# Kernel tuning notes

Measured on AMD Instinct MI355X. Metric: run time of the kernel, lower is better.

Reference implementation:

```python
import jax, jax.numpy as jnp
import numpy as np

N_NODES = 50000


def gcn_conv(x, W, b, src, dst, n):
    """PyG GCNConv: add self-loops, sym-normalize, linear, scatter-add."""
    loop = jnp.arange(n, dtype=src.dtype)
    s = jnp.concatenate([src, loop])  # [E+N]
    d = jnp.concatenate([dst, loop])
    deg = jax.ops.segment_sum(jnp.ones_like(s, dtype=x.dtype), d, num_segments=n)
    dinv = jnp.where(deg > 0, jax.lax.rsqrt(deg), 0.0)  # deg^-1/2
    norm = dinv[s] * dinv[d]  # [E+N]
    h = x @ W  # [N, out] dense GEMM first (in >= out)
    msg = h[s] * norm[:, None]  # gather + scale
    out = jax.ops.segment_sum(msg, d, num_segments=n)  # scatter-add
    return out + b


def setup_inputs() -> dict:
    key = jax.random.key(0)
    k1, k2, k3, k4, k5, k6, k7, k8 = jax.random.split(key, 8)
    in_c, hid_c, out_c = 512, 128, 64
    n, e, l = N_NODES, 800000, 100000
    x = jax.random.normal(k1, (n, in_c), dtype=jnp.float32)
    edge_index = jax.random.randint(k2, (2, e), 0, n, dtype=jnp.int64)
    edge_label_index = jax.random.randint(k3, (2, l), 0, n, dtype=jnp.int64)
    # Glorot-ish init for weights, zeros for biases (PyG default bias=zeros)
    W1 = jax.random.normal(k4, (in_c, hid_c), dtype=jnp.float32) / np.sqrt(in_c)
    b1 = jnp.zeros((hid_c,), dtype=jnp.float32)
    W2 = jax.random.normal(k5, (hid_c, out_c), dtype=jnp.float32) / np.sqrt(hid_c)
    b2 = jnp.zeros((out_c,), dtype=jnp.float32)
    return {"x": x, "edge_index": edge_index, "edge_label_index": edge_label_index,
            "W1": W1, "b1": b1, "W2": W2, "b2": b2}


def reference(x, edge_index, edge_label_index, W1, b1, W2, b2):
    n = x.shape[0]
    src, dst = edge_index[0], edge_index[1]
    z = jax.nn.relu(gcn_conv(x, W1, b1, src, dst, n))
    z = gcn_conv(z, W2, b2, src, dst, n)
    es, ed = edge_label_index[0], edge_label_index[1]
    return jnp.sum(z[es] * z[ed], axis=-1).reshape(-1)
```

## Files before the change

kernel.cpp:

```cpp
#include <hip/hip_runtime.h>

#define IN_C  512
#define HID_C 128
#define OUT_C 64

using short8 = __attribute__((ext_vector_type(8))) short;
using floatx4 = __attribute__((ext_vector_type(4))) float;

__device__ inline unsigned short f2bf(float f) {
    unsigned u = __builtin_bit_cast(unsigned, f);
    u += 0x7FFFu + ((u >> 16) & 1u);
    return (unsigned short)(u >> 16);
}
__device__ inline float bf2f(unsigned short h) {
    unsigned u = ((unsigned)h) << 16;
    return __builtin_bit_cast(float, u);
}

__global__ void k_zero_int(int* __restrict__ p, int n) {
    int i = blockIdx.x * blockDim.x + threadIdx.x;
    if (i < n) p[i] = 0;
}

__global__ void k_count(const int* __restrict__ dst, int* __restrict__ cnt, int e) {
    int i = blockIdx.x * blockDim.x + threadIdx.x;
    if (i < e) atomicAdd(&cnt[dst[i]], 1);
}

__global__ void k_dinv(const int* __restrict__ cnt, float* __restrict__ dinv, int n) {
    int i = blockIdx.x * blockDim.x + threadIdx.x;
    if (i < n) dinv[i] = rsqrtf(1.0f + (float)cnt[i]);
}

__global__ void k_blocksum(const int* __restrict__ cnt, int* __restrict__ bsum, int n) {
    __shared__ int sdata[256];
    int t = threadIdx.x;
    int i = blockIdx.x * 256 + t;
    sdata[t] = (i < n) ? cnt[i] : 0;
    __syncthreads();
    for (int s = 128; s > 0; s >>= 1) {
        if (t < s) sdata[t] += sdata[t + s];
        __syncthreads();
    }
    if (t == 0) bsum[blockIdx.x] = sdata[0];
}

__global__ void k_scanpartials(int* __restrict__ bsum, int nb) {
    __shared__ int sdata[256];
    int t = threadIdx.x;
    int orig = (t < nb) ? bsum[t] : 0;
    sdata[t] = orig;
    __syncthreads();
    for (int off = 1; off < 256; off <<= 1) {
        int v = (t >= off) ? sdata[t - off] : 0;
        __syncthreads();
        sdata[t] += v;
        __syncthreads();
    }
    if (t < nb) bsum[t] = sdata[t] - orig;
}

__global__ void k_scanfinal(const int* __restrict__ cnt, const int* __restrict__ bsum_ex,
                            int* __restrict__ row_ptr, int n, int e_total) {
    __shared__ int sdata[256];
    int t = threadIdx.x;
    int i = blockIdx.x * 256 + t;
    int orig = (i < n) ? cnt[i] : 0;
    sdata[t] = orig;
    __syncthreads();
    for (int off = 1; off < 256; off <<= 1) {
        int v = (t >= off) ? sdata[t - off] : 0;
        __syncthreads();
        sdata[t] += v;
        __syncthreads();
    }
    if (i < n) row_ptr[i] = sdata[t] - orig + bsum_ex[blockIdx.x];
    if (i == 0) row_ptr[n] = e_total;
}

__global__ void k_fill(const int* __restrict__ src, const int* __restrict__ dst,
                       const int* __restrict__ row_ptr, int* __restrict__ cur,
                       int* __restrict__ col, int e) {
    int i = blockIdx.x * blockDim.x + threadIdx.x;
    if (i < e) {
        int d = dst[i];
        int pos = atomicAdd(&cur[d], 1);
        col[row_ptr[d] + pos] = src[i];
    }
}

__global__ void k_prep_w(const float* __restrict__ W, unsigned short* __restrict__ hi,
                         unsigned short* __restrict__ lo, int K, int N) {
    int i = blockIdx.x * blockDim.x + threadIdx.x;
    if (i >= K * N) return;
    int k = i / N, n = i % N;
    float v = W[i];
    unsigned short h = f2bf(v);
    float r = v - bf2f(h);
    hi[(long)n * K + k] = h;
    lo[(long)n * K + k] = f2bf(r);
}

template <int K, int NPW, int BM>
__global__ __launch_bounds__(256) void k_gemm_mfma(
    const float* __restrict__ A, const unsigned short* __restrict__ Bt_hi,
    const unsigned short* __restrict__ Bt_lo, const float* __restrict__ dinv,
    float* __restrict__ Hs, int M) {
    constexpr int N = 64 * NPW;
    constexpr int LDA = 72;
    constexpr int NT = K / 64;
    constexpr int MI = BM / 16;
    __shared__ __align__(16) unsigned short As_hi[2][BM * LDA];
    __shared__ __align__(16) unsigned short As_lo[2][BM * LDA];

    const int tid = threadIdx.x;
    const int w = tid >> 6;
    const int lane = tid & 63;
    const int m = lane & 15;
    const int quad = lane >> 4;
    const int m0 = blockIdx.x * BM;

    const int srow = tid >> 4;
    const int skk = (tid & 15) << 2;

    floatx4 acc[MI][NPW];
#pragma unroll
    for (int mi = 0; mi < MI; ++mi)
#pragma unroll
        for (int ni = 0; ni < NPW; ++ni) acc[mi][ni] = (floatx4){0.f, 0.f, 0.f, 0.f};

    float4 pf[MI];
#pragma unroll
    for (int i = 0; i < MI; ++i) {
        int gm = m0 + srow + 16 * i;
        pf[i] = make_float4(0.f, 0.f, 0.f, 0.f);
        if (gm < M) pf[i] = *(const float4*)&A[(long)gm * K + skk];
    }
#pragma unroll
    for (int i = 0; i < MI; ++i) {
        ushort4 h, l;
        h.x = f2bf(pf[i].x); l.x = f2bf(pf[i].x - bf2f(h.x));
        h.y = f2bf(pf[i].y); l.y = f2bf(pf[i].y - bf2f(h.y));
        h.z = f2bf(pf[i].z); l.z = f2bf(pf[i].z - bf2f(h.z));
        h.w = f2bf(pf[i].w); l.w = f2bf(pf[i].w - bf2f(h.w));
        int off = (srow + 16 * i) * LDA + skk;
        *(ushort4*)&As_hi[0][off] = h;
        *(ushort4*)&As_lo[0][off] = l;
    }

    for (int t = 0; t < NT; ++t) {
        __syncthreads();
        const int buf = t & 1;
        if (t + 1 < NT) {
#pragma unroll
            for (int i = 0; i < MI; ++i) {
                int gm = m0 + srow + 16 * i;
                pf[i] = make_float4(0.f, 0.f, 0.f, 0.f);
                if (gm < M) pf[i] = *(const float4*)&A[(long)gm * K + (t + 1) * 64 + skk];
            }
        }
#pragma unroll
        for (int s = 0; s < 2; ++s) {
            short8 ah[MI], al[MI];
#pragma unroll
            for (int mi = 0; mi < MI; ++mi) {
                int off = (mi * 16 + m) * LDA + s * 32 + quad * 8;
                ah[mi] = *(const short8*)&As_hi[buf][off];
                al[mi] = *(const short8*)&As_lo[buf][off];
            }
#pragma unroll
            for (int ni = 0; ni < NPW; ++ni) {
                int n = (w * NPW + ni) * 16 + m;
                long boff = (long)n * K + t * 64 + s * 32 + quad * 8;
                short8 bh = *(const short8*)&Bt_hi[boff];
                short8 bl = *(const short8*)&Bt_lo[boff];
#pragma unroll
                for (int mi = 0; mi < MI; ++mi) {
                    acc[mi][ni] = __builtin_amdgcn_mfma_f32_16x16x32_bf16(ah[mi], bh, acc[mi][ni], 0, 0, 0);
                    acc[mi][ni] = __builtin_amdgcn_mfma_f32_16x16x32_bf16(ah[mi], bl, acc[mi][ni], 0, 0, 0);
                    acc[mi][ni] = __builtin_amdgcn_mfma_f32_16x16x32_bf16(al[mi], bh, acc[mi][ni], 0, 0, 0);
                }
            }
        }
        if (t + 1 < NT) {
#pragma unroll
            for (int i = 0; i < MI; ++i) {
                ushort4 h, l;
                h.x = f2bf(pf[i].x); l.x = f2bf(pf[i].x - bf2f(h.x));
                h.y = f2bf(pf[i].y); l.y = f2bf(pf[i].y - bf2f(h.y));
                h.z = f2bf(pf[i].z); l.z = f2bf(pf[i].z - bf2f(h.z));
                h.w = f2bf(pf[i].w); l.w = f2bf(pf[i].w - bf2f(h.w));
                int off = (srow + 16 * i) * LDA + skk;
                *(ushort4*)&As_hi[buf ^ 1][off] = h;
                *(ushort4*)&As_lo[buf ^ 1][off] = l;
            }
        }
    }

#pragma unroll
    for (int mi = 0; mi < MI; ++mi) {
#pragma unroll
        for (int r = 0; r < 4; ++r) {
            int row = m0 + mi * 16 + quad * 4 + r;
            if (row < M) {
                float dv = dinv[row];
#pragma unroll
                for (int ni = 0; ni < NPW; ++ni) {
                    int n = (w * NPW + ni) * 16 + m;
                    Hs[(long)row * N + n] = acc[mi][ni][r] * dv;
                }
            }
        }
    }
}

__global__ __launch_bounds__(256) void k_agg1(
    const float* __restrict__ h, const int* __restrict__ row_ptr,
    const int* __restrict__ col, const float* __restrict__ dinv,
    const float* __restrict__ bias, float* __restrict__ z, int n) {
    int node = blockIdx.x * 4 + (threadIdx.x >> 6);
    node = __builtin_amdgcn_readfirstlane(node);
    if (node >= n) return;
    int lane = threadIdx.x & 63;
    const float2* hp = (const float2*)h;
    float2 acc = hp[(long)node * 64 + lane];
    int rs = row_ptr[node], re = row_ptr[node + 1];
    int j = rs;
    for (; j + 4 <= re; j += 4) {
        int s0 = col[j], s1 = col[j + 1], s2 = col[j + 2], s3 = col[j + 3];
        float2 v0 = hp[(long)s0 * 64 + lane];
        float2 v1 = hp[(long)s1 * 64 + lane];
        float2 v2 = hp[(long)s2 * 64 + lane];
        float2 v3 = hp[(long)s3 * 64 + lane];
        acc.x += v0.x + v1.x + v2.x + v3.x;
        acc.y += v0.y + v1.y + v2.y + v3.y;
    }
    for (; j < re; ++j) {
        int s = col[j];
        float2 v = hp[(long)s * 64 + lane];
        acc.x += v.x;
        acc.y += v.y;
    }
    float dv = dinv[node];
    float2 b = ((const float2*)bias)[lane];
    acc.x = fmaxf(fmaf(acc.x, dv, b.x), 0.f);
    acc.y = fmaxf(fmaf(acc.y, dv, b.y), 0.f);
    ((float2*)z)[(long)node * 64 + lane] = acc;
}

__global__ __launch_bounds__(256) void k_agg2(
    const float* __restrict__ h, const int* __restrict__ row_ptr,
    const int* __restrict__ col, const float* __restrict__ dinv,
    const float* __restrict__ bias, float* __restrict__ z, int n) {
    int node = blockIdx.x * 4 + (threadIdx.x >> 6);
    node = __builtin_amdgcn_readfirstlane(node);
    if (node >= n) return;
    int lane = threadIdx.x & 63;
    float acc = h[(long)node * 64 + lane];
    int rs = row_ptr[node], re = row_ptr[node + 1];
    int j = rs;
    for (; j + 4 <= re; j += 4) {
        int s0 = col[j], s1 = col[j + 1], s2 = col[j + 2], s3 = col[j + 3];
        acc += h[(long)s0 * 64 + lane] + h[(long)s1 * 64 + lane] +
               h[(long)s2 * 64 + lane] + h[(long)s3 * 64 + lane];
    }
    for (; j < re; ++j) acc += h[(long)col[j] * 64 + lane];
    z[(long)node * 64 + lane] = fmaf(acc, dinv[node], bias[lane]);
}

__global__ void k_dot(const float* __restrict__ z2, const int* __restrict__ es,
                      const int* __restrict__ ed, float* __restrict__ out, int L) {
    int gid = blockIdx.x * blockDim.x + threadIdx.x;
    int wid = gid >> 6;
    int lane = threadIdx.x & 63;
    if (wid >= L) return;
    int a = es[wid], b = ed[wid];
    float v = z2[(long)a * OUT_C + lane] * z2[(long)b * OUT_C + lane];
#pragma unroll
    for (int off = 32; off > 0; off >>= 1) v += __shfl_down(v, off);
    if (lane == 0) out[wid] = v;
}

extern "C" void kernel_launch(void* const* d_in, const int* in_sizes, int n_in,
                              void* d_out, int out_size, void* d_ws, size_t ws_size,
                              hipStream_t stream) {
    const float* x = (const float*)d_in[0];
    const int* ei = (const int*)d_in[1];
    const int* eli = (const int*)d_in[2];
    const float* W1 = (const float*)d_in[3];
    const float* b1 = (const float*)d_in[4];
    const float* W2 = (const float*)d_in[5];
    const float* b2 = (const float*)d_in[6];
    float* out = (float*)d_out;

    const int N = in_sizes[0] / IN_C;
    const int E = in_sizes[1] / 2;
    const int L = in_sizes[2] / 2;
    const int* src = ei;
    const int* dst = ei + E;
    const int* es = eli;
    const int* ed = eli + L;

    const int Npad = (N + 63) & ~63;
    const int Epad = (E + 3) & ~3;

    int* cnt = (int*)d_ws;
    int* cur = cnt + Npad;
    int* row_ptr = cur + Npad;
    int* bsum = row_ptr + Npad + 64;
    int* col = bsum + 256;
    float* dinv = (float*)(col + Epad);
    float* h1s = dinv + Npad;
    float* z1 = h1s + (long)N * HID_C;
    float* h2s = h1s;
    float* z2 = h1s + (long)N * OUT_C;
    unsigned short* wt1_hi = (unsigned short*)(z1 + (long)N * HID_C);
    unsigned short* wt1_lo = wt1_hi + IN_C * HID_C;
    unsigned short* wt2_hi = wt1_lo + IN_C * HID_C;
    unsigned short* wt2_lo = wt2_hi + HID_C * OUT_C;

    const int TPB = 256;
    const int nb = (N + 255) / 256;

    k_prep_w<<<(IN_C * HID_C + TPB - 1) / TPB, TPB, 0, stream>>>(W1, wt1_hi, wt1_lo, IN_C, HID_C);
    k_prep_w<<<(HID_C * OUT_C + TPB - 1) / TPB, TPB, 0, stream>>>(W2, wt2_hi, wt2_lo, HID_C, OUT_C);

    k_zero_int<<<(2 * Npad + TPB - 1) / TPB, TPB, 0, stream>>>(cnt, 2 * Npad);
    k_count<<<(E + TPB - 1) / TPB, TPB, 0, stream>>>(dst, cnt, E);
    k_dinv<<<(N + TPB - 1) / TPB, TPB, 0, stream>>>(cnt, dinv, N);
    k_blocksum<<<nb, 256, 0, stream>>>(cnt, bsum, N);
    k_scanpartials<<<1, 256, 0, stream>>>(bsum, nb);
    k_scanfinal<<<nb, 256, 0, stream>>>(cnt, bsum, row_ptr, N, E);
    k_fill<<<(E + TPB - 1) / TPB, TPB, 0, stream>>>(src, dst, row_ptr, cur, col, E);

    k_gemm_mfma<IN_C, 2, 32><<<(N + 31) / 32, 256, 0, stream>>>(x, wt1_hi, wt1_lo, dinv, h1s, N);
    k_agg1<<<(N + 3) / 4, 256, 0, stream>>>(h1s, row_ptr, col, dinv, b1, z1, N);

    k_gemm_mfma<HID_C, 1, 32><<<(N + 31) / 32, 256, 0, stream>>>(z1, wt2_hi, wt2_lo, dinv, h2s, N);
    k_agg2<<<(N + 3) / 4, 256, 0, stream>>>(h2s, row_ptr, col, dinv, b2, z2, N);

    k_dot<<<((long)L * 64 + TPB - 1) / TPB, TPB, 0, stream>>>(z2, es, ed, out, L);
}
```

Measured before the change: 418.9 us.

## Load GEMM A operands directly into registers, dropping LDS staging and barriers

Replaces the LDS-staged, double-buffered GEMM with a version where each wave loads its A fragment straight from global memory into registers (floatx8 per lane), splits it into bf16 hi/lo in place, and prefetches two k-steps ahead. The aim is to remove shared-memory traffic and __syncthreads from the memory-bound x@W1 GEMM. Block tiling also changes to 64 rows per block with a 2x2 or 4x1 wave grid. In exchange, A rows are re-read by every wave that shares them, which puts more pressure on cache. Out-of-range rows are clamped rather than zero-filled.

```diff
diff --git a/kernel.cpp b/kernel.cpp
--- a/kernel.cpp
+++ b/kernel.cpp
@@ -6,6 +6,7 @@
 
 using short8 = __attribute__((ext_vector_type(8))) short;
 using floatx4 = __attribute__((ext_vector_type(4))) float;
+using floatx8 = __attribute__((ext_vector_type(8))) float;
 
 __device__ inline unsigned short f2bf(float f) {
     unsigned u = __builtin_bit_cast(unsigned, f);
@@ -101,27 +102,37 @@
     lo[(long)n * K + k] = f2bf(r);
 }
 
-template <int K, int NPW, int BM>
-__global__ __launch_bounds__(256) void k_gemm_mfma(
+template <int K, int MI, int NPW, int WM, int WN>
+__global__ __launch_bounds__(256) void k_gemm_direct(
     const float* __restrict__ A, const unsigned short* __restrict__ Bt_hi,
     const unsigned short* __restrict__ Bt_lo, const float* __restrict__ dinv,
     float* __restrict__ Hs, int M) {
-    constexpr int N = 64 * NPW;
-    constexpr int LDA = 72;
-    constexpr int NT = K / 64;
-    constexpr int MI = BM / 16;
-    __shared__ __align__(16) unsigned short As_hi[2][BM * LDA];
-    __shared__ __align__(16) unsigned short As_lo[2][BM * LDA];
+    constexpr int N = WN * NPW * 16;
+    constexpr int BM = WM * MI * 16;
+    constexpr int NT = K / 32;
 
     const int tid = threadIdx.x;
     const int w = tid >> 6;
     const int lane = tid & 63;
+    const int wm = w / WN;
+    const int wn = w % WN;
     const int m = lane & 15;
     const int quad = lane >> 4;
-    const int m0 = blockIdx.x * BM;
-
-    const int srow = tid >> 4;
-    const int skk = (tid & 15) << 2;
+    const int rowbase = blockIdx.x * BM + wm * (MI * 16);
+    const int colbase = wn * (NPW * 16);
+    const int koff = quad * 8;
+
+    long aoff[MI];
+#pragma unroll
+    for (int mi = 0; mi < MI; ++mi) {
+        int r = rowbase + mi * 16 + m;
+        if (r > M - 1) r = M - 1;
+        aoff[mi] = (long)r * K + koff;
+    }
+    long boff[NPW];
+#pragma unroll
+    for (int ni = 0; ni < NPW; ++ni)
+        boff[ni] = (long)(colbase + ni * 16 + m) * K + koff;
 
     floatx4 acc[MI][NPW];
 #pragma unroll
@@ -129,84 +140,55 @@
 #pragma unroll
         for (int ni = 0; ni < NPW; ++ni) acc[mi][ni] = (floatx4){0.f, 0.f, 0.f, 0.f};
 
-    float4 pf[MI];
-#pragma unroll
-    for (int i = 0; i < MI; ++i) {
-        int gm = m0 + srow + 16 * i;
-        pf[i] = make_float4(0.f, 0.f, 0.f, 0.f);
-        if (gm < M) pf[i] = *(const float4*)&A[(long)gm * K + skk];
-    }
-#pragma unroll
-    for (int i = 0; i < MI; ++i) {
-        ushort4 h, l;
-        h.x = f2bf(pf[i].x); l.x = f2bf(pf[i].x - bf2f(h.x));
-        h.y = f2bf(pf[i].y); l.y = f2bf(pf[i].y - bf2f(h.y));
-        h.z = f2bf(pf[i].z); l.z = f2bf(pf[i].z - bf2f(h.z));
-        h.w = f2bf(pf[i].w); l.w = f2bf(pf[i].w - bf2f(h.w));
-        int off = (srow + 16 * i) * LDA + skk;
-        *(ushort4*)&As_hi[0][off] = h;
-        *(ushort4*)&As_lo[0][off] = l;
-    }
-
+    floatx8 pf[2][MI];
+#pragma unroll
+    for (int mi = 0; mi < MI; ++mi) pf[0][mi] = *(const floatx8*)&A[aoff[mi]];
+    if (NT > 1) {
+#pragma unroll
+        for (int mi = 0; mi < MI; ++mi) pf[1][mi] = *(const floatx8*)&A[aoff[mi] + 32];
+    }
+
+#pragma unroll
     for (int t = 0; t < NT; ++t) {
-        __syncthreads();
-        const int buf = t & 1;
-        if (t + 1 < NT) {
-#pragma unroll
-            for (int i = 0; i < MI; ++i) {
-                int gm = m0 + srow + 16 * i;
-                pf[i] = make_float4(0.f, 0.f, 0.f, 0.f);
-                if (gm < M) pf[i] = *(const float4*)&A[(long)gm * K + (t + 1) * 64 + skk];
+        short8 ah[MI], al[MI];
+#pragma unroll
+        for (int mi = 0; mi < MI; ++mi) {
+            floatx8 v = pf[t & 1][mi];
+#pragma unroll
+            for (int j = 0; j < 8; ++j) {
+                unsigned short h = f2bf(v[j]);
+                ah[mi][j] = (short)h;
+                al[mi][j] = (short)f2bf(v[j] - bf2f(h));
             }
         }
-#pragma unroll
-        for (int s = 0; s < 2; ++s) {
-            short8 ah[MI], al[MI];
+        if (t + 2 < NT) {
+#pragma unroll
+            for (int mi = 0; mi < MI; ++mi)
+                pf[t & 1][mi] = *(const floatx8*)&A[aoff[mi] + (t + 2) * 32];
+        }
+#pragma unroll
+        for (int ni = 0; ni < NPW; ++ni) {
+            short8 bh = *(const short8*)&Bt_hi[boff[ni] + t * 32];
+            short8 bl = *(const short8*)&Bt_lo[boff[ni] + t * 32];
 #pragma unroll
             for (int mi = 0; mi < MI; ++mi) {
-                int off = (mi * 16 + m) * LDA + s * 32 + quad * 8;
-                ah[mi] = *(const short8*)&As_hi[buf][off];
-                al[mi] = *(const short8*)&As_lo[buf][off];
-            }
-#pragma unroll
-            for (int ni = 0; ni < NPW; ++ni) {
-                int n = (w * NPW + ni) * 16 + m;
-                long boff = (long)n * K + t * 64 + s * 32 + quad * 8;
-                short8 bh = *(const short8*)&Bt_hi[boff];
-                short8 bl = *(const short8*)&Bt_lo[boff];
-#pragma unroll
-                for (int mi = 0; mi < MI; ++mi) {
-                    acc[mi][ni] = __builtin_amdgcn_mfma_f32_16x16x32_bf16(ah[mi], bh, acc[mi][ni], 0, 0, 0);
-                    acc[mi][ni] = __builtin_amdgcn_mfma_f32_16x16x32_bf16(ah[mi], bl, acc[mi][ni], 0, 0, 0);
-                    acc[mi][ni] = __builtin_amdgcn_mfma_f32_16x16x32_bf16(al[mi], bh, acc[mi][ni], 0, 0, 0);
-                }
+                acc[mi][ni] = __builtin_amdgcn_mfma_f32_16x16x32_bf16(ah[mi], bh, acc[mi][ni], 0, 0, 0);
+                acc[mi][ni] = __builtin_amdgcn_mfma_f32_16x16x32_bf16(ah[mi], bl, acc[mi][ni], 0, 0, 0);
+                acc[mi][ni] = __builtin_amdgcn_mfma_f32_16x16x32_bf16(al[mi], bh, acc[mi][ni], 0, 0, 0);
             }
         }
-        if (t + 1 < NT) {
-#pragma unroll
-            for (int i = 0; i < MI; ++i) {
-                ushort4 h, l;
-                h.x = f2bf(pf[i].x); l.x = f2bf(pf[i].x - bf2f(h.x));
-                h.y = f2bf(pf[i].y); l.y = f2bf(pf[i].y - bf2f(h.y));
-                h.z = f2bf(pf[i].z); l.z = f2bf(pf[i].z - bf2f(h.z));
-                h.w = f2bf(pf[i].w); l.w = f2bf(pf[i].w - bf2f(h.w));
-                int off = (srow + 16 * i) * LDA + skk;
-                *(ushort4*)&As_hi[buf ^ 1][off] = h;
-                *(ushort4*)&As_lo[buf ^ 1][off] = l;
-            }
-        }
     }
 
 #pragma unroll
     for (int mi = 0; mi < MI; ++mi) {
 #pragma unroll
         for (int r = 0; r < 4; ++r) {
-            int row = m0 + mi * 16 + quad * 4 + r;
+            int row = rowbase + mi * 16 + quad * 4 + r;
             if (row < M) {
                 float dv = dinv[row];
 #pragma unroll
                 for (int ni = 0; ni < NPW; ++ni) {
-                    int n = (w * NPW + ni) * 16 + m;
+                    int n = colbase + ni * 16 + m;
                     Hs[(long)row * N + n] = acc[mi][ni][r] * dv;
                 }
             }
@@ -333,10 +315,10 @@
     k_scanfinal<<<nb, 256, 0, stream>>>(cnt, bsum, row_ptr, N, E);
     k_fill<<<(E + TPB - 1) / TPB, TPB, 0, stream>>>(src, dst, row_ptr, cur, col, E);
 
-    k_gemm_mfma<IN_C, 2, 32><<<(N + 31) / 32, 256, 0, stream>>>(x, wt1_hi, wt1_lo, dinv, h1s, N);
+    k_gemm_direct<IN_C, 2, 4, 2, 2><<<(N + 63) / 64, 256, 0, stream>>>(x, wt1_hi, wt1_lo, dinv, h1s, N);
     k_agg1<<<(N + 3) / 4, 256, 0, stream>>>(h1s, row_ptr, col, dinv, b1, z1, N);
 
-    k_gemm_mfma<HID_C, 1, 32><<<(N + 31) / 32, 256, 0, stream>>>(z1, wt2_hi, wt2_lo, dinv, h2s, N);
+    k_gemm_direct<HID_C, 1, 4, 4, 1><<<(N + 63) / 64, 256, 0, stream>>>(z1, wt2_hi, wt2_lo, dinv, h2s, N);
     k_agg2<<<(N + 3) / 4, 256, 0, stream>>>(h2s, row_ptr, col, dinv, b2, z2, N);
 
     k_dot<<<((long)L * 64 + TPB - 1) / TPB, TPB, 0, stream>>>(z2, es, ed, out, L);
```

Result: slower. 450.8 us (+7.6%).
